# Kernel optimization log

Hardware: AMD Instinct MI355X
Metric: run time of the kernel (lower is better)

The kernel has to match this reference:

```python
import jax, jax.numpy as jnp
import numpy as np

B, S, H, UNITS = 32, 2048, 1024, 1024

def setup_inputs() -> dict:
    key = jax.random.key(0)
    ks = jax.random.split(key, 8)
    sc_h = 1.0 / np.sqrt(H)
    sc_u = 1.0 / np.sqrt(UNITS)
    return {
        "query": jax.random.normal(ks[0], (B, H), jnp.float32),
        "values": jax.random.normal(ks[1], (B, S, H), jnp.float32),
        "W1": jax.random.normal(ks[2], (H, UNITS), jnp.float32) * sc_h,
        "b1": jnp.zeros((UNITS,), jnp.float32),
        "W2": jax.random.normal(ks[3], (H, UNITS), jnp.float32) * sc_h,
        "b2": jnp.zeros((UNITS,), jnp.float32),
        "V": jax.random.normal(ks[4], (UNITS, 1), jnp.float32) * sc_u,
        "bv": jnp.zeros((1,), jnp.float32),
    }

def reference(query, values, W1, b1, W2, b2, V, bv):
    # W1(values): [B,S,U]; W2(query)[:,None,:]: [B,1,U] broadcast-added
    proj = jnp.tanh(
        jnp.einsum("bsh,hu->bsu", values, W1) + b1
        + (query @ W2 + b2)[:, None, :]
    )
    score = proj @ V + bv                      # [B,S,1]
    attention_weights = jax.nn.softmax(score, axis=1)  # softmax over seq
    context_vector = jnp.sum(attention_weights * values, axis=1)  # [B,H]
    return context_vector, attention_weights
```

## Files before the change

### kernel.cpp

```cpp
#include <hip/hip_runtime.h>
#include <hip/hip_bf16.h>


#define B_ 32
#define S_ 2048
#define H_ 1024
#define U_ 1024
#define M_ (B_ * S_)

typedef __bf16 bf16;
typedef __bf16 bf16x8 __attribute__((ext_vector_type(8)));
typedef float  f32x4  __attribute__((ext_vector_type(4)));

__device__ __forceinline__ void gl2lds16(const void* g, void* l) {
    __builtin_amdgcn_global_load_lds(
        (const __attribute__((address_space(1))) void*)g,
        (__attribute__((address_space(3))) void*)l, 16, 0, 0);
}

__global__ void transpose_w1(const float* __restrict__ W1, bf16* __restrict__ W1T) {
    __shared__ bf16 t[64 * 65];
    int h0 = blockIdx.x * 64, u0 = blockIdx.y * 64;
    int tid = threadIdx.x;
    #pragma unroll
    for (int i = 0; i < 16; ++i) {
        int idx = i * 256 + tid;
        int r = idx >> 6, c = idx & 63;
        t[c * 65 + r] = (bf16)W1[(long)(h0 + r) * U_ + u0 + c];
    }
    __syncthreads();
    #pragma unroll
    for (int i = 0; i < 16; ++i) {
        int idx = i * 256 + tid;
        int r = idx >> 6, c = idx & 63;
        W1T[(long)(u0 + r) * H_ + h0 + c] = t[r * 65 + c];
    }
}

__global__ void q2_kernel(const float* __restrict__ query, const float* __restrict__ W2,
                          const float* __restrict__ b2, float* __restrict__ q2) {
    __shared__ float qsh[H_];
    __shared__ float part[4][64];
    int b = blockIdx.y;
    int u0 = blockIdx.x * 64;
    int tid = threadIdx.x;
    int ul = tid & 63, kc = tid >> 6;
    for (int i = tid; i < H_; i += 256) qsh[i] = query[b * H_ + i];
    __syncthreads();
    float acc = 0.f;
    const float* wp = W2 + (long)(kc * 256) * U_ + u0 + ul;
    #pragma unroll 8
    for (int h = 0; h < 256; ++h) acc += qsh[kc * 256 + h] * wp[(long)h * U_];
    part[kc][ul] = acc;
    __syncthreads();
    if (tid < 64)
        q2[b * U_ + u0 + tid] = part[0][tid] + part[1][tid] + part[2][tid] + part[3][tid]
                                + b2[u0 + tid];
}

__global__ __launch_bounds__(256, 3) void score_gemm(
    const float* __restrict__ A32,
    const bf16* __restrict__ BT,
    const float* __restrict__ b1, const float* __restrict__ q2,
    const float* __restrict__ V, float* __restrict__ score )
{
    __shared__ __align__(16) float a_sh[2 * 128 * 32];
    __shared__ __align__(16) bf16  b_sh[2 * 128 * 32];
    const int tid  = threadIdx.x;
    const int lane = tid & 63;
    const int wave = tid >> 6;
    const int wm = wave >> 1, wn = wave & 1;
    const int xcd = blockIdx.x & 7;
    const int i_  = blockIdx.x >> 3;
    const int nt  = i_ & 7;
    const int mt  = xcd * 64 + (i_ >> 3);
    const long m0 = (long)mt * 128;
    const int  n0 = nt * 128;
    const int lrow = lane & 15;
    const int quad = lane >> 4;

    f32x4 acc[4][4];
    const f32x4 zero = {0.f, 0.f, 0.f, 0.f};
    #pragma unroll
    for (int mi = 0; mi < 4; ++mi)
        #pragma unroll
        for (int ni = 0; ni < 4; ++ni) acc[mi][ni] = zero;

    const float* Abase = A32 + m0 * H_;
    const bf16*  Bbase = BT + (long)n0 * H_;

    for (int kt = 0; kt < H_; kt += 64) {
        #pragma unroll
        for (int i = 0; i < 8; ++i) {
            int g  = i * 4 + wave;
            int hs = g >> 4, q = g & 15;
            int row = q * 8 + (lane >> 3);
            int gc  = (lane & 7) ^ (row & 7);
            gl2lds16(Abase + (long)row * H_ + kt + hs * 32 + gc * 4,
                     (void*)(a_sh + hs * 4096 + q * 256));
        }
        #pragma unroll
        for (int i = 0; i < 4; ++i) {
            int g  = i * 4 + wave;
            int hs = g >> 3, q = g & 7;
            int row = q * 16 + (lane >> 2);
            int gc  = (lane & 3) ^ ((row >> 1) & 3);
            gl2lds16(Bbase + (long)row * H_ + kt + hs * 32 + gc * 8,
                     (void*)(b_sh + hs * 4096 + q * 512));
        }
        __syncthreads();

        #pragma unroll
        for (int hs = 0; hs < 2; ++hs) {
            bf16x8 af[4], bg[4];
            #pragma unroll
            for (int mi = 0; mi < 4; ++mi) {
                int r  = wm * 64 + mi * 16 + lrow;
                int p0 = (2 * quad) ^ (r & 7);
                const float4 lo = *reinterpret_cast<const float4*>(
                    a_sh + hs * 4096 + r * 32 + p0 * 4);
                const float4 hi = *reinterpret_cast<const float4*>(
                    a_sh + hs * 4096 + r * 32 + (p0 ^ 1) * 4);
                bf16x8 f;
                f[0] = (bf16)lo.x; f[1] = (bf16)lo.y; f[2] = (bf16)lo.z; f[3] = (bf16)lo.w;
                f[4] = (bf16)hi.x; f[5] = (bf16)hi.y; f[6] = (bf16)hi.z; f[7] = (bf16)hi.w;
                af[mi] = f;
            }
            #pragma unroll
            for (int ni = 0; ni < 4; ++ni) {
                int r = wn * 64 + ni * 16 + lrow;
                int p = quad ^ ((r >> 1) & 3);
                bg[ni] = *reinterpret_cast<const bf16x8*>(
                    b_sh + hs * 4096 + r * 32 + p * 8);
            }
            #pragma unroll
            for (int mi = 0; mi < 4; ++mi)
                #pragma unroll
                for (int ni = 0; ni < 4; ++ni)
                    acc[mi][ni] = __builtin_amdgcn_mfma_f32_16x16x32_bf16(
                        af[mi], bg[ni], acc[mi][ni], 0, 0, 0);
        }
        __syncthreads();
    }

    const int bb = (int)(m0 / S_);
    float bq[4], vv[4];
    #pragma unroll
    for (int ni = 0; ni < 4; ++ni) {
        int u = n0 + wn * 64 + ni * 16 + lrow;
        bq[ni] = b1[u] + q2[bb * U_ + u];
        vv[ni] = V[u];
    }
    #pragma unroll
    for (int mi = 0; mi < 4; ++mi) {
        #pragma unroll
        for (int r = 0; r < 4; ++r) {
            float s = 0.f;
            #pragma unroll
            for (int ni = 0; ni < 4; ++ni) {
                float x = acc[mi][ni][r] + bq[ni];
                float t = 1.f - 2.f / (__expf(2.f * x) + 1.f);
                s += t * vv[ni];
            }
            s += __shfl_xor(s, 1); s += __shfl_xor(s, 2);
            s += __shfl_xor(s, 4); s += __shfl_xor(s, 8);
            if (lrow == 0)
                atomicAdd(score + m0 + wm * 64 + mi * 16 + quad * 4 + r, s);
        }
    }
}

__global__ void softmax_kernel(float* __restrict__ attn) {
    __shared__ float sh[S_];
    __shared__ float red[8];
    int b = blockIdx.x, tid = threadIdx.x;
    float* row = attn + (long)b * S_;
    float lmax = -1e30f;
    for (int i = tid; i < S_; i += 256) { float v = row[i]; sh[i] = v; lmax = fmaxf(lmax, v); }
    #pragma unroll
    for (int m = 32; m; m >>= 1) lmax = fmaxf(lmax, __shfl_xor(lmax, m));
    if ((tid & 63) == 0) red[tid >> 6] = lmax;
    __syncthreads();
    float gmax = fmaxf(fmaxf(red[0], red[1]), fmaxf(red[2], red[3]));
    float lsum = 0.f;
    for (int i = tid; i < S_; i += 256) { float e = __expf(sh[i] - gmax); sh[i] = e; lsum += e; }
    #pragma unroll
    for (int m = 32; m; m >>= 1) lsum += __shfl_xor(lsum, m);
    if ((tid & 63) == 0) red[4 + (tid >> 6)] = lsum;
    __syncthreads();
    float inv = 1.f / (red[4] + red[5] + red[6] + red[7]);
    for (int i = tid; i < S_; i += 256) row[i] = sh[i] * inv;
}

__global__ void context_kernel(const float* __restrict__ vals, const float* __restrict__ attn,
                               float* __restrict__ ctx ) {
    __shared__ float a_sh[128];
    int b = blockIdx.x >> 4;
    int sc = blockIdx.x & 15;
    int tid = threadIdx.x;
    if (tid < 128) a_sh[tid] = attn[(long)b * S_ + sc * 128 + tid];
    __syncthreads();
    const float* base = vals + ((long)b * S_ + sc * 128) * H_ + tid * 4;
    float ax = 0.f, ay = 0.f, az = 0.f, aw = 0.f;
    #pragma unroll 4
    for (int s = 0; s < 128; ++s) {
        float w = a_sh[s];
        float4 v = *reinterpret_cast<const float4*>(base + (long)s * H_);
        ax += w * v.x; ay += w * v.y; az += w * v.z; aw += w * v.w;
    }
    float* c = ctx + (long)b * H_ + tid * 4;
    atomicAdd(c + 0, ax); atomicAdd(c + 1, ay);
    atomicAdd(c + 2, az); atomicAdd(c + 3, aw);
}

extern "C" void kernel_launch(void* const* d_in, const int* in_sizes, int n_in,
                              void* d_out, int out_size, void* d_ws, size_t ws_size,
                              hipStream_t stream) {
    const float* query  = (const float*)d_in[0];
    const float* values = (const float*)d_in[1];
    const float* W1     = (const float*)d_in[2];
    const float* b1     = (const float*)d_in[3];
    const float* W2     = (const float*)d_in[4];
    const float* b2     = (const float*)d_in[5];
    const float* V      = (const float*)d_in[6];

    char* ws = (char*)d_ws;
    bf16*  w1t = (bf16*)ws;
    float* q2  = (float*)(ws + (size_t)U_ * H_ * 2);

    float* ctx  = (float*)d_out;
    float* attn = (float*)d_out + B_ * H_;

    hipMemsetAsync(d_out, 0, (size_t)(B_ * H_ + B_ * S_) * sizeof(float), stream);

    transpose_w1  <<<dim3(16, 16),       256, 0, stream>>>(W1, w1t);
    q2_kernel     <<<dim3(U_ / 64, B_),  256, 0, stream>>>(query, W2, b2, q2);
    score_gemm    <<<(M_ / 128) * 8,     256, 0, stream>>>(values, w1t, b1, q2, V, attn);
    softmax_kernel<<<B_,                 256, 0, stream>>>(attn);
    context_kernel<<<B_ * 16,            256, 0, stream>>>(values, attn, ctx);
}
```

Baseline: 605.2 us.

## Convert A tile to bf16 on load and merge prep kernels into one launch

The score GEMM now loads fp32 activation tiles through registers, converts them to bf16 once, and stores them in a padded bf16 LDS layout. This replaces the async global-to-LDS fp32 copy that was converted repeatedly inside the MFMA loop. The change halves LDS footprint and read traffic for A and removes redundant conversions. The cost is that the direct async LDS load for A is lost, so global load latency may be less hidden. Separately, the W1 transpose and the query projection are fused into a single prep kernel to save one launch.

```diff
diff --git a/kernel.cpp b/kernel.cpp
--- a/kernel.cpp
+++ b/kernel.cpp
@@ -18,54 +18,64 @@
         (__attribute__((address_space(3))) void*)l, 16, 0, 0);
 }
 
-__global__ void transpose_w1(const float* __restrict__ W1, bf16* __restrict__ W1T) {
-    __shared__ bf16 t[64 * 65];
-    int h0 = blockIdx.x * 64, u0 = blockIdx.y * 64;
+__device__ __forceinline__ bf16x8 cvt8(float4 a, float4 b) {
+    bf16x8 o;
+    o[0] = (bf16)a.x; o[1] = (bf16)a.y; o[2] = (bf16)a.z; o[3] = (bf16)a.w;
+    o[4] = (bf16)b.x; o[5] = (bf16)b.y; o[6] = (bf16)b.z; o[7] = (bf16)b.w;
+    return o;
+}
+
+__global__ void prep_kernel(const float* __restrict__ W1, bf16* __restrict__ W1T,
+                            const float* __restrict__ query, const float* __restrict__ W2,
+                            const float* __restrict__ b2, float* __restrict__ q2) {
+    __shared__ __align__(16) char smem[64 * 65 * 2];
     int tid = threadIdx.x;
-    #pragma unroll
-    for (int i = 0; i < 16; ++i) {
-        int idx = i * 256 + tid;
-        int r = idx >> 6, c = idx & 63;
-        t[c * 65 + r] = (bf16)W1[(long)(h0 + r) * U_ + u0 + c];
-    }
-    __syncthreads();
-    #pragma unroll
-    for (int i = 0; i < 16; ++i) {
-        int idx = i * 256 + tid;
-        int r = idx >> 6, c = idx & 63;
-        W1T[(long)(u0 + r) * H_ + h0 + c] = t[r * 65 + c];
-    }
-}
-
-__global__ void q2_kernel(const float* __restrict__ query, const float* __restrict__ W2,
-                          const float* __restrict__ b2, float* __restrict__ q2) {
-    __shared__ float qsh[H_];
-    __shared__ float part[4][64];
-    int b = blockIdx.y;
-    int u0 = blockIdx.x * 64;
-    int tid = threadIdx.x;
-    int ul = tid & 63, kc = tid >> 6;
-    for (int i = tid; i < H_; i += 256) qsh[i] = query[b * H_ + i];
-    __syncthreads();
-    float acc = 0.f;
-    const float* wp = W2 + (long)(kc * 256) * U_ + u0 + ul;
-    #pragma unroll 8
-    for (int h = 0; h < 256; ++h) acc += qsh[kc * 256 + h] * wp[(long)h * U_];
-    part[kc][ul] = acc;
-    __syncthreads();
-    if (tid < 64)
-        q2[b * U_ + u0 + tid] = part[0][tid] + part[1][tid] + part[2][tid] + part[3][tid]
-                                + b2[u0 + tid];
-}
-
+    if (blockIdx.x < 256) {
+        bf16* t = (bf16*)smem;
+        int h0 = (blockIdx.x >> 4) * 64, u0 = (blockIdx.x & 15) * 64;
+        #pragma unroll
+        for (int i = 0; i < 16; ++i) {
+            int idx = i * 256 + tid;
+            int r = idx >> 6, c = idx & 63;
+            t[c * 65 + r] = (bf16)W1[(long)(h0 + r) * U_ + u0 + c];
+        }
+        __syncthreads();
+        #pragma unroll
+        for (int i = 0; i < 16; ++i) {
+            int idx = i * 256 + tid;
+            int r = idx >> 6, c = idx & 63;
+            W1T[(long)(u0 + r) * H_ + h0 + c] = t[r * 65 + c];
+        }
+    } else {
+        float* qsh  = (float*)smem;
+        float* part = (float*)(smem + 4096);
+        int idx = blockIdx.x - 256;
+        int b  = idx >> 4;
+        int u0 = (idx & 15) * 64;
+        int ul = tid & 63, kc = tid >> 6;
+        for (int i = tid; i < H_; i += 256) qsh[i] = query[b * H_ + i];
+        __syncthreads();
+        float acc = 0.f;
+        const float* wp = W2 + (long)(kc * 256) * U_ + u0 + ul;
+        #pragma unroll 8
+        for (int h = 0; h < 256; ++h) acc += qsh[kc * 256 + h] * wp[(long)h * U_];
+        part[kc * 64 + ul] = acc;
+        __syncthreads();
+        if (tid < 64)
+            q2[b * U_ + u0 + tid] = part[tid] + part[64 + tid] + part[128 + tid]
+                                    + part[192 + tid] + b2[u0 + tid];
+    }
+}
+
+#define ASTRIDE 40
 __global__ __launch_bounds__(256, 3) void score_gemm(
     const float* __restrict__ A32,
     const bf16* __restrict__ BT,
     const float* __restrict__ b1, const float* __restrict__ q2,
     const float* __restrict__ V, float* __restrict__ score )
 {
-    __shared__ __align__(16) float a_sh[2 * 128 * 32];
-    __shared__ __align__(16) bf16  b_sh[2 * 128 * 32];
+    __shared__ __align__(16) bf16 a_sh[2 * 128 * ASTRIDE];
+    __shared__ __align__(16) bf16 b_sh[2 * 128 * 32];
     const int tid  = threadIdx.x;
     const int lane = tid & 63;
     const int wave = tid >> 6;
@@ -78,6 +88,8 @@
     const int  n0 = nt * 128;
     const int lrow = lane & 15;
     const int quad = lane >> 4;
+    const int arow = tid >> 1;
+    const int aseg = tid & 1;
 
     f32x4 acc[4][4];
     const f32x4 zero = {0.f, 0.f, 0.f, 0.f};
@@ -90,15 +102,6 @@
     const bf16*  Bbase = BT + (long)n0 * H_;
 
     for (int kt = 0; kt < H_; kt += 64) {
-        #pragma unroll
-        for (int i = 0; i < 8; ++i) {
-            int g  = i * 4 + wave;
-            int hs = g >> 4, q = g & 15;
-            int row = q * 8 + (lane >> 3);
-            int gc  = (lane & 7) ^ (row & 7);
-            gl2lds16(Abase + (long)row * H_ + kt + hs * 32 + gc * 4,
-                     (void*)(a_sh + hs * 4096 + q * 256));
-        }
         #pragma unroll
         for (int i = 0; i < 4; ++i) {
             int g  = i * 4 + wave;
@@ -108,6 +111,20 @@
             gl2lds16(Bbase + (long)row * H_ + kt + hs * 32 + gc * 8,
                      (void*)(b_sh + hs * 4096 + q * 512));
         }
+        float4 av[2][4];
+        #pragma unroll
+        for (int hs = 0; hs < 2; ++hs) {
+            const float4* src = reinterpret_cast<const float4*>(
+                Abase + (long)arow * H_ + kt + hs * 32 + aseg * 16);
+            av[hs][0] = src[0]; av[hs][1] = src[1];
+            av[hs][2] = src[2]; av[hs][3] = src[3];
+        }
+        #pragma unroll
+        for (int hs = 0; hs < 2; ++hs) {
+            bf16* dst = a_sh + hs * (128 * ASTRIDE) + arow * ASTRIDE + aseg * 16;
+            *reinterpret_cast<bf16x8*>(dst)     = cvt8(av[hs][0], av[hs][1]);
+            *reinterpret_cast<bf16x8*>(dst + 8) = cvt8(av[hs][2], av[hs][3]);
+        }
         __syncthreads();
 
         #pragma unroll
@@ -115,16 +132,9 @@
             bf16x8 af[4], bg[4];
             #pragma unroll
             for (int mi = 0; mi < 4; ++mi) {
-                int r  = wm * 64 + mi * 16 + lrow;
-                int p0 = (2 * quad) ^ (r & 7);
-                const float4 lo = *reinterpret_cast<const float4*>(
-                    a_sh + hs * 4096 + r * 32 + p0 * 4);
-                const float4 hi = *reinterpret_cast<const float4*>(
-                    a_sh + hs * 4096 + r * 32 + (p0 ^ 1) * 4);
-                bf16x8 f;
-                f[0] = (bf16)lo.x; f[1] = (bf16)lo.y; f[2] = (bf16)lo.z; f[3] = (bf16)lo.w;
-                f[4] = (bf16)hi.x; f[5] = (bf16)hi.y; f[6] = (bf16)hi.z; f[7] = (bf16)hi.w;
-                af[mi] = f;
+                int r = wm * 64 + mi * 16 + lrow;
+                af[mi] = *reinterpret_cast<const bf16x8*>(
+                    a_sh + hs * (128 * ASTRIDE) + r * ASTRIDE + quad * 8);
             }
             #pragma unroll
             for (int ni = 0; ni < 4; ++ni) {
@@ -233,9 +243,8 @@
 
     hipMemsetAsync(d_out, 0, (size_t)(B_ * H_ + B_ * S_) * sizeof(float), stream);
 
-    transpose_w1  <<<dim3(16, 16),       256, 0, stream>>>(W1, w1t);
-    q2_kernel     <<<dim3(U_ / 64, B_),  256, 0, stream>>>(query, W2, b2, q2);
-    score_gemm    <<<(M_ / 128) * 8,     256, 0, stream>>>(values, w1t, b1, q2, V, attn);
-    softmax_kernel<<<B_,                 256, 0, stream>>>(attn);
-    context_kernel<<<B_ * 16,            256, 0, stream>>>(values, attn, ctx);
-}
+    prep_kernel   <<<768,            256, 0, stream>>>(W1, w1t, query, W2, b2, q2);
+    score_gemm    <<<(M_ / 128) * 8, 256, 0, stream>>>(values, w1t, b1, q2, V, attn);
+    softmax_kernel<<<B_,             256, 0, stream>>>(attn);
+    context_kernel<<<B_ * 16,        256, 0, stream>>>(values, attn, ctx);
+}
```

Result: no change. 596.9 us (-1.4%).
